# Kernel optimization log

Measured on AMD Instinct MI355X. Metric: run time of the kernel, lower is better.

## Reference

```python
import jax, jax.numpy as jnp
import numpy as np

B, S, D = 2, 2048, 1024
NH, HD = 16, 64
MLP = 4096
EPS = 1e-6  # flax nnx.RMSNorm default epsilon


def rms_norm(x, scale):
    var = jnp.mean(jnp.square(x.astype(jnp.float32)), axis=-1, keepdims=True)
    return (x * jax.lax.rsqrt(var + EPS)).astype(x.dtype) * scale


def setup_inputs() -> dict:
    key = jax.random.key(0)
    ks = jax.random.split(key, 16)
    lin = lambda k, fin, fout: jax.random.normal(k, (fin, fout), jnp.float32) / np.sqrt(fin)
    x = jax.random.normal(ks[0], (B, S, D), jnp.float32)
    # causal mask [b, s, s]
    mask = jnp.broadcast_to(jnp.tril(jnp.ones((S, S), jnp.bool_))[None], (B, S, S))
    return {
        "x": x,
        "mask": mask,
        "attn_norm_scale": jnp.ones((D,), jnp.float32),
        "q_w": lin(ks[1], D, D), "q_b": jnp.zeros((D,), jnp.float32),
        "k_w": lin(ks[2], D, D), "k_b": jnp.zeros((D,), jnp.float32),
        "v_w": lin(ks[3], D, D), "v_b": jnp.zeros((D,), jnp.float32),
        "o_w": lin(ks[4], D, D), "o_b": jnp.zeros((D,), jnp.float32),
        "ffn_norm_scale": jnp.ones((D,), jnp.float32),
        "gate_w": lin(ks[5], D, MLP), "gate_b": jnp.zeros((MLP,), jnp.float32),
        "up_w": lin(ks[6], D, MLP), "up_b": jnp.zeros((MLP,), jnp.float32),
        "down_w": lin(ks[7], MLP, D), "down_b": jnp.zeros((D,), jnp.float32),
    }


def reference(x, mask, attn_norm_scale, q_w, q_b, k_w, k_b, v_w, v_b, o_w, o_b,
              ffn_norm_scale, gate_w, gate_b, up_w, up_b, down_w, down_b):
    b, s, d = x.shape
    h = rms_norm(x, attn_norm_scale)
    q = (h @ q_w + q_b).reshape(b, s, NH, HD)
    k = (h @ k_w + k_b).reshape(b, s, NH, HD)
    v = (h @ v_w + v_b).reshape(b, s, NH, HD)
    scale = jnp.float32(HD) ** -0.5
    logits = jnp.einsum('bsnh,btnh->bnst', q, k) * scale  # [b, n, s, s]
    logits = jnp.where(mask[:, None, :, :], logits, jnp.finfo(logits.dtype).min)
    attn = jax.nn.softmax(logits.astype(jnp.float32), axis=-1).astype(x.dtype)
    attn_out = jnp.einsum('bnst,btnh->bsnh', attn, v).reshape(b, s, d)
    x = x + attn_out @ o_w + o_b
    h = rms_norm(x, ffn_norm_scale)
    ffn = (jax.nn.silu(h @ gate_w + gate_b) * (h @ up_w + up_b)) @ down_w + down_b
    return x + ffn
```

## Files before the change

kernel.cpp:

```cpp
#include <hip/hip_runtime.h>

#define S_LEN 2048
#define DMODEL 1024
#define NHEADS 16
#define MLPDIM 4096

typedef float f32x4 __attribute__((ext_vector_type(4)));
typedef __bf16 bf16x8 __attribute__((ext_vector_type(8)));
typedef __bf16 bf16x4 __attribute__((ext_vector_type(4)));

__device__ __forceinline__ void gload_lds16(const void* gsrc, void* ldst) {
  __builtin_amdgcn_global_load_lds(
      (const __attribute__((address_space(1))) void*)gsrc,
      (__attribute__((address_space(3))) void*)ldst, 16, 0, 0);
}

#define BARR() __builtin_amdgcn_s_barrier()
#define VMC(n) do { asm volatile("s_waitcnt vmcnt(" #n ")" ::: "memory"); __builtin_amdgcn_sched_barrier(0); } while (0)

__global__ __launch_bounds__(256) void transpose_cast64_k(
    const float* __restrict__ in, __bf16* __restrict__ out, int K, int N) {
  __shared__ __bf16 tile[64][66];
  int n0 = blockIdx.x * 64, k0 = blockIdx.y * 64;
  int t = threadIdx.x;
  int rr = (t & 63) >> 4, sl = t & 15, wv = t >> 6;
#pragma unroll
  for (int j = 0; j < 4; ++j) {
    int r = wv * 4 + rr + j * 16;
    f32x4 v = *(const f32x4*)(in + (size_t)(k0 + r) * N + n0 + sl * 4);
#pragma unroll
    for (int e = 0; e < 4; ++e) tile[r][sl * 4 + e] = (__bf16)v[e];
  }
  __syncthreads();
#pragma unroll
  for (int j = 0; j < 2; ++j) {
    int u = t + j * 256;
    int n = u >> 3, kc = u & 7;
    bf16x8 o;
#pragma unroll
    for (int e = 0; e < 8; ++e) o[e] = tile[kc * 8 + e][n];
    *(bf16x8*)(out + (size_t)(n0 + n) * K + k0 + kc * 8) = o;
  }
}

__global__ __launch_bounds__(256) void vtrans_k(
    const __bf16* __restrict__ qkv, __bf16* __restrict__ vt) {
  __shared__ __bf16 tile[32][33];
  int s0 = blockIdx.x * 32, c0 = blockIdx.y * 32, b = blockIdx.z;
  int tx = threadIdx.x & 31, ty = threadIdx.x >> 5;
#pragma unroll
  for (int r = 0; r < 32; r += 8)
    tile[r + ty][tx] = qkv[(size_t)(b * S_LEN + s0 + r + ty) * 3072 + 2048 + c0 + tx];
  __syncthreads();
#pragma unroll
  for (int r = 0; r < 32; r += 8)
    vt[(size_t)(b * 1024 + c0 + r + ty) * S_LEN + s0 + tx] = tile[tx][r + ty];
}

__global__ __launch_bounds__(256) void concat3_k(
    const float* __restrict__ a, const float* __restrict__ b,
    const float* __restrict__ c, float* __restrict__ dst) {
  int i = blockIdx.x * 256 + threadIdx.x;
  if (i < 1024) dst[i] = a[i];
  else if (i < 2048) dst[i] = b[i - 1024];
  else if (i < 3072) dst[i] = c[i - 2048];
}

__global__ __launch_bounds__(256) void rmsnorm_k(
    const float* __restrict__ x, const float* __restrict__ scale,
    __bf16* __restrict__ out) {
  int row = blockIdx.x, tid = threadIdx.x;
  f32x4 v = ((const f32x4*)(x + (size_t)row * DMODEL))[tid];
  float ss = v[0] * v[0] + v[1] * v[1] + v[2] * v[2] + v[3] * v[3];
#pragma unroll
  for (int off = 1; off < 64; off <<= 1) ss += __shfl_xor(ss, off, 64);
  __shared__ float part[4];
  if ((tid & 63) == 0) part[tid >> 6] = ss;
  __syncthreads();
  float tot = part[0] + part[1] + part[2] + part[3];
  float r = rsqrtf(tot * (1.0f / DMODEL) + 1e-6f);
  f32x4 s4 = ((const f32x4*)scale)[tid];
  bf16x4 o;
#pragma unroll
  for (int e = 0; e < 4; ++e) o[e] = (__bf16)(v[e] * r * s4[e]);
  ((bf16x4*)out)[(size_t)row * (DMODEL / 4) + tid] = o;
}

__global__ __launch_bounds__(256, 4) void gemm_gu(
    const __bf16* __restrict__ A, const __bf16* __restrict__ Gt,
    const __bf16* __restrict__ Ut, const float* __restrict__ gb,
    const float* __restrict__ ub, __bf16* __restrict__ Cout,
    int M, int N, int K) {
  __shared__ __attribute__((aligned(16))) __bf16 As[128 * 64];
  __shared__ __attribute__((aligned(16))) __bf16 Gs[64 * 64];
  __shared__ __attribute__((aligned(16))) __bf16 Us[64 * 64];
  int tid = threadIdx.x, lane = tid & 63, wave = tid >> 6;
  int l15 = lane & 15, g4 = lane >> 4;
  int lin = blockIdx.x;
  int xcd = lin & 7, idx = lin >> 3;
  int bxl = idx >> 4, byl = idx & 15;
  int bn = ((xcd & 3) * 16 + bxl) * 64;
  int bm = ((xcd >> 2) * 16 + byl) * 128;
  int wr = wave >> 1, wc = wave & 1;
  f32x4 ag[4][2] = {}, au[4][2] = {};
  const __bf16* Abase = A + (size_t)bm * K;
  const __bf16* Gbase = Gt + (size_t)bn * K;
  const __bf16* Ubase = Ut + (size_t)bn * K;

  for (int k0 = 0; k0 < K; k0 += 64) {
#pragma unroll
    for (int j = 0; j < 4; ++j) {
      int u = tid + j * 256;
      int r = u >> 3, c = (u & 7) ^ (r & 7);
      gload_lds16(Abase + (size_t)r * K + k0 + c * 8, As + u * 8);
    }
#pragma unroll
    for (int j = 0; j < 2; ++j) {
      int u = tid + j * 256;
      int r = u >> 3, c = (u & 7) ^ (r & 7);
      gload_lds16(Gbase + (size_t)r * K + k0 + c * 8, Gs + u * 8);
      gload_lds16(Ubase + (size_t)r * K + k0 + c * 8, Us + u * 8);
    }
    __syncthreads();
#pragma unroll
    for (int ks = 0; ks < 2; ++ks) {
      bf16x8 af[4], gf[2], uf[2];
#pragma unroll
      for (int m = 0; m < 4; ++m) {
        int r = wr * 64 + m * 16 + l15;
        af[m] = *(const bf16x8*)(As + r * 64 + (((4 * ks + g4) ^ (r & 7)) << 3));
      }
#pragma unroll
      for (int n = 0; n < 2; ++n) {
        int r = wc * 32 + n * 16 + l15;
        int off = r * 64 + (((4 * ks + g4) ^ (r & 7)) << 3);
        gf[n] = *(const bf16x8*)(Gs + off);
        uf[n] = *(const bf16x8*)(Us + off);
      }
      __builtin_amdgcn_s_setprio(1);
#pragma unroll
      for (int m = 0; m < 4; ++m)
#pragma unroll
        for (int n = 0; n < 2; ++n) {
          ag[m][n] = __builtin_amdgcn_mfma_f32_16x16x32_bf16(af[m], gf[n], ag[m][n], 0, 0, 0);
          au[m][n] = __builtin_amdgcn_mfma_f32_16x16x32_bf16(af[m], uf[n], au[m][n], 0, 0, 0);
        }
      __builtin_amdgcn_s_setprio(0);
    }
    __syncthreads();
  }
  int r0 = bm + wr * 64 + g4 * 4;
  int c0 = bn + wc * 32 + l15;
#pragma unroll
  for (int n = 0; n < 2; ++n) {
    int c = c0 + n * 16;
    float gbv = gb[c], ubv = ub[c];
#pragma unroll
    for (int m = 0; m < 4; ++m) {
      int rb = r0 + m * 16;
#pragma unroll
      for (int rg = 0; rg < 4; ++rg) {
        float g = ag[m][n][rg] + gbv;
        float u = au[m][n][rg] + ubv;
        float v = g / (1.0f + __expf(-g)) * u;
        Cout[(size_t)(rb + rg) * N + c] = (__bf16)v;
      }
    }
  }
}

template <int OUT_BF16, int RESID, int SILU>
__global__ __launch_bounds__(256, 3) void gemm_n64(
    const __bf16* __restrict__ A, const __bf16* __restrict__ Bt,
    const float* __restrict__ bias, const float* __restrict__ resid,
    const __bf16* __restrict__ aux, void* __restrict__ Cout,
    int M, int N, int K) {
  __shared__ __attribute__((aligned(16))) __bf16 As[2][128 * 64];
  __shared__ __attribute__((aligned(16))) __bf16 Bs[2][64 * 64];
  int tid = threadIdx.x, lane = tid & 63, wave = tid >> 6;
  int l15 = lane & 15, g4 = lane >> 4;
  int npx = M >> 10;
  int xcd = blockIdx.x & 7, j = blockIdx.x >> 3;
  int bm = (xcd * npx + (j % npx)) * 128;
  int bn = (j / npx) * 64;
  int wr = wave >> 1, wc = wave & 1;
  f32x4 acc[4][2] = {};
  const __bf16* Abase = A + (size_t)bm * K;
  const __bf16* Bbase = Bt + (size_t)bn * K;

  auto stage = [&](int k0, int sb) {
#pragma unroll
    for (int i = 0; i < 4; ++i) {
      int u = tid + i * 256;
      int r = u >> 3, c = (u & 7) ^ (r & 7);
      gload_lds16(Abase + (size_t)r * K + k0 + c * 8, As[sb] + u * 8);
    }
#pragma unroll
    for (int i = 0; i < 2; ++i) {
      int u = tid + i * 256;
      int r = u >> 3, c = (u & 7) ^ (r & 7);
      gload_lds16(Bbase + (size_t)r * K + k0 + c * 8, Bs[sb] + u * 8);
    }
  };

  int NT = K >> 6;
  stage(0, 0);
  for (int t = 0; t < NT; ++t) {
    int sb = t & 1;
    if (t + 1 < NT) { stage((t + 1) << 6, sb ^ 1); VMC(6); }
    else { VMC(0); }
    BARR();
#pragma unroll
    for (int ks = 0; ks < 2; ++ks) {
      bf16x8 af[4], bfr[2];
#pragma unroll
      for (int m = 0; m < 4; ++m) {
        int r = wr * 64 + m * 16 + l15;
        af[m] = *(const bf16x8*)(As[sb] + r * 64 + (((4 * ks + g4) ^ (r & 7)) << 3));
      }
#pragma unroll
      for (int n = 0; n < 2; ++n) {
        int r = wc * 32 + n * 16 + l15;
        bfr[n] = *(const bf16x8*)(Bs[sb] + r * 64 + (((4 * ks + g4) ^ (r & 7)) << 3));
      }
      __builtin_amdgcn_s_setprio(1);
#pragma unroll
      for (int m = 0; m < 4; ++m)
#pragma unroll
        for (int n = 0; n < 2; ++n)
          acc[m][n] = __builtin_amdgcn_mfma_f32_16x16x32_bf16(af[m], bfr[n], acc[m][n], 0, 0, 0);
      __builtin_amdgcn_s_setprio(0);
    }
    BARR();
  }
  int r0 = bm + wr * 64 + g4 * 4;
  int c0 = bn + wc * 32 + l15;
#pragma unroll
  for (int n = 0; n < 2; ++n) {
    int c = c0 + n * 16;
    float bv = bias[c];
#pragma unroll
    for (int m = 0; m < 4; ++m) {
      int rb = r0 + m * 16;
#pragma unroll
      for (int rg = 0; rg < 4; ++rg) {
        int r = rb + rg;
        size_t idx = (size_t)r * N + c;
        float v = acc[m][n][rg] + bv;
        if (SILU) {
          float gg = (float)aux[idx];
          v *= gg / (1.0f + __expf(-gg));
        }
        if (RESID) v += resid[idx];
        if (OUT_BF16) ((__bf16*)Cout)[idx] = (__bf16)v;
        else ((float*)Cout)[idx] = v;
      }
    }
  }
}

#define SCL2E 0.180336879f
__global__ __launch_bounds__(512, 4) void attn_k(
    const __bf16* __restrict__ qkv, const __bf16* __restrict__ vt,
    __bf16* __restrict__ ao) {
  __shared__ __attribute__((aligned(16))) __bf16 Ks[2][128 * 64];
  __shared__ __attribute__((aligned(16))) __bf16 Vs[2][64 * 128];
  int tid = threadIdx.x, lane = tid & 63, w = tid >> 6;
  int l15 = lane & 15, g4 = lane >> 4;
  int bh = blockIdx.x, b = bh >> 4, h = bh & 15;
  int qt = 15 - blockIdx.y;
  int qb = qt * 128;
  int qw = qb + w * 16;
  const __bf16* qkvb = qkv + (size_t)b * S_LEN * 3072 + h * 64;
  const __bf16* kgb = qkvb + 1024;
  const __bf16* vtb = vt + (size_t)b * 1024 * S_LEN + (size_t)(h * 64) * S_LEN;

  bf16x8 qf[2];
#pragma unroll
  for (int ks = 0; ks < 2; ++ks)
    qf[ks] = *(const bf16x8*)(qkvb + (size_t)(qw + l15) * 3072 + 32 * ks + 8 * g4);

  f32x4 oa[4] = {};
  float mrow = -1e30f, lrow = 0.f;
  int q = qw + l15;
  int nt = qt + 1;

  auto stage = [&](int kvb, int buf) {
#pragma unroll
    for (int i = 0; i < 2; ++i) {
      int u = tid + i * 512;
      int r = u >> 3, c = u & 7;
      gload_lds16(kgb + (size_t)(kvb + r) * 3072 + ((c ^ (r & 7)) << 3),
                  Ks[buf] + w * 512 + i * 4096);
    }
#pragma unroll
    for (int i = 0; i < 2; ++i) {
      int u = tid + i * 512;
      int r = u >> 4, cu = u & 15;
      gload_lds16(vtb + (size_t)r * S_LEN + kvb + ((cu ^ (r & 7)) << 3),
                  Vs[buf] + w * 512 + i * 4096);
    }
  };

  stage(0, 0);
  __syncthreads();
  int buf = 0;
  for (int t = 0; t < nt; ++t) {
    int kvb = t * 128;
    if (t + 1 < nt) stage(kvb + 128, buf ^ 1);

    f32x4 sa[8];
#pragma unroll
    for (int i = 0; i < 8; ++i) sa[i] = f32x4{0.f, 0.f, 0.f, 0.f};
#pragma unroll
    for (int st = 0; st < 2; ++st)
#pragma unroll
      for (int ks = 0; ks < 2; ++ks) {
        bf16x8 kf[4];
#pragma unroll
        for (int n = 0; n < 4; ++n) {
          int rr = st * 64 + n * 16 + l15;
          int bc = (64 * ks + 16 * g4) ^ ((rr & 7) << 4);
          kf[n] = *(const bf16x8*)((const char*)Ks[buf] + rr * 128 + bc);
        }
        __builtin_amdgcn_s_setprio(1);
#pragma unroll
        for (int n = 0; n < 4; ++n)
          sa[st * 4 + n] = __builtin_amdgcn_mfma_f32_16x16x32_bf16(kf[n], qf[ks], sa[st * 4 + n], 0, 0, 0);
        __builtin_amdgcn_s_setprio(0);
      }

    bool lastt = (t == nt - 1);
    float nmx = -1e30f;
#pragma unroll
    for (int i = 0; i < 8; ++i)
#pragma unroll
      for (int rg = 0; rg < 4; ++rg) {
        float s = sa[i][rg] * SCL2E;
        if (lastt) {
          int key = kvb + (i >> 2) * 64 + (i & 3) * 16 + 4 * g4 + rg;
          s = (key <= q) ? s : -1e30f;
        }
        sa[i][rg] = s;
        nmx = fmaxf(nmx, s);
      }
    nmx = fmaxf(nmx, __shfl_xor(nmx, 16));
    nmx = fmaxf(nmx, __shfl_xor(nmx, 32));
    float nm = fmaxf(mrow, nmx);
    float sc = exp2f(mrow - nm);
    mrow = nm;
    float rs = 0.f;
    bf16x8 pa[2][2];
#pragma unroll
    for (int st = 0; st < 2; ++st)
#pragma unroll
      for (int ks = 0; ks < 2; ++ks)
#pragma unroll
        for (int hf = 0; hf < 2; ++hf)
#pragma unroll
          for (int rg = 0; rg < 4; ++rg) {
            float p = exp2f(sa[st * 4 + 2 * ks + hf][rg] - nm);
            rs += p;
            pa[st][ks][hf * 4 + rg] = (__bf16)p;
          }
    rs += __shfl_xor(rs, 16);
    rs += __shfl_xor(rs, 32);
    lrow = lrow * sc + rs;
#pragma unroll
    for (int rg = 0; rg < 4; ++rg) {
      float scq = __shfl(sc, 4 * g4 + rg);
#pragma unroll
      for (int dn = 0; dn < 4; ++dn) oa[dn][rg] *= scq;
    }

#pragma unroll
    for (int st = 0; st < 2; ++st)
#pragma unroll
      for (int ks = 0; ks < 2; ++ks) {
        __builtin_amdgcn_s_setprio(1);
#pragma unroll
        for (int dn = 0; dn < 4; ++dn) {
          int rr = dn * 16 + l15;
          int swz = (rr & 7) << 4;
          int bb = st * 128 + 64 * ks + 8 * g4;
          const char* vrow = (const char*)Vs[buf] + rr * 256;
          bf16x4 v0 = *(const bf16x4*)(vrow + (bb ^ swz));
          bf16x4 v1 = *(const bf16x4*)(vrow + ((bb + 32) ^ swz));
          bf16x8 vf;
          vf[0] = v0[0]; vf[1] = v0[1]; vf[2] = v0[2]; vf[3] = v0[3];
          vf[4] = v1[0]; vf[5] = v1[1]; vf[6] = v1[2]; vf[7] = v1[3];
          oa[dn] = __builtin_amdgcn_mfma_f32_16x16x32_bf16(pa[st][ks], vf, oa[dn], 0, 0, 0);
        }
        __builtin_amdgcn_s_setprio(0);
      }
    __syncthreads();
    buf ^= 1;
  }

  __bf16* aobase = ao + (size_t)b * S_LEN * DMODEL + h * 64;
#pragma unroll
  for (int rg = 0; rg < 4; ++rg) {
    float rl = 1.0f / __shfl(lrow, 4 * g4 + rg);
    int qo = qw + 4 * g4 + rg;
#pragma unroll
    for (int dn = 0; dn < 4; ++dn)
      aobase[(size_t)qo * DMODEL + dn * 16 + l15] = (__bf16)(oa[dn][rg] * rl);
  }
}

#define OFF_WQKV 0
#define OFF_WO 6291456
#define OFF_WG 8388608
#define OFF_WU 16777216
#define OFF_WD 25165824
#define OFF_BQKV 33554432
#define OFF_H 33570816
#define OFF_QKV 41959424
#define OFF_AO 67125248
#define OFF_T 75513856
#define OFF_VT OFF_T
#define OFF_X2 109068288

extern "C" void kernel_launch(void* const* d_in, const int* in_sizes, int n_in,
                              void* d_out, int out_size, void* d_ws, size_t ws_size,
                              hipStream_t stream) {
  (void)in_sizes; (void)n_in; (void)out_size; (void)ws_size;
  const float* x = (const float*)d_in[0];
  const float* attn_scale = (const float*)d_in[2];
  const float* q_w = (const float*)d_in[3];
  const float* q_b = (const float*)d_in[4];
  const float* k_w = (const float*)d_in[5];
  const float* k_b = (const float*)d_in[6];
  const float* v_w = (const float*)d_in[7];
  const float* v_b = (const float*)d_in[8];
  const float* o_w = (const float*)d_in[9];
  const float* o_b = (const float*)d_in[10];
  const float* ffn_scale = (const float*)d_in[11];
  const float* gate_w = (const float*)d_in[12];
  const float* gate_b = (const float*)d_in[13];
  const float* up_w = (const float*)d_in[14];
  const float* up_b = (const float*)d_in[15];
  const float* down_w = (const float*)d_in[16];
  const float* down_b = (const float*)d_in[17];

  char* ws = (char*)d_ws;
  __bf16* wqkv = (__bf16*)(ws + OFF_WQKV);
  __bf16* wo = (__bf16*)(ws + OFF_WO);
  __bf16* wg = (__bf16*)(ws + OFF_WG);
  __bf16* wu = (__bf16*)(ws + OFF_WU);
  __bf16* wd = (__bf16*)(ws + OFF_WD);
  float* bqkv = (float*)(ws + OFF_BQKV);
  __bf16* hbuf = (__bf16*)(ws + OFF_H);
  __bf16* qkvbuf = (__bf16*)(ws + OFF_QKV);
  __bf16* aobuf = (__bf16*)(ws + OFF_AO);
  __bf16* tbuf = (__bf16*)(ws + OFF_T);
  __bf16* vtbuf = (__bf16*)(ws + OFF_VT);
  float* x2 = (float*)(ws + OFF_X2);

  dim3 blk(256);
  transpose_cast64_k<<<dim3(16, 16), blk, 0, stream>>>(q_w, wqkv, 1024, 1024);
  transpose_cast64_k<<<dim3(16, 16), blk, 0, stream>>>(k_w, wqkv + 1024 * 1024, 1024, 1024);
  transpose_cast64_k<<<dim3(16, 16), blk, 0, stream>>>(v_w, wqkv + 2 * 1024 * 1024, 1024, 1024);
  transpose_cast64_k<<<dim3(16, 16), blk, 0, stream>>>(o_w, wo, 1024, 1024);
  transpose_cast64_k<<<dim3(64, 16), blk, 0, stream>>>(gate_w, wg, 1024, 4096);
  transpose_cast64_k<<<dim3(64, 16), blk, 0, stream>>>(up_w, wu, 1024, 4096);
  transpose_cast64_k<<<dim3(16, 64), blk, 0, stream>>>(down_w, wd, 4096, 1024);
  concat3_k<<<12, blk, 0, stream>>>(q_b, k_b, v_b, bqkv);
  rmsnorm_k<<<4096, blk, 0, stream>>>(x, attn_scale, hbuf);
  gemm_n64<1, 0, 0><<<dim3(1536), blk, 0, stream>>>(hbuf, wqkv, bqkv, nullptr, nullptr, qkvbuf, 4096, 3072, 1024);
  vtrans_k<<<dim3(64, 32, 2), blk, 0, stream>>>(qkvbuf, vtbuf);
  attn_k<<<dim3(32, 16), dim3(512), 0, stream>>>(qkvbuf, vtbuf, aobuf);
  gemm_n64<0, 1, 0><<<dim3(512), blk, 0, stream>>>(aobuf, wo, o_b, x, nullptr, x2, 4096, 1024, 1024);
  rmsnorm_k<<<4096, blk, 0, stream>>>(x2, ffn_scale, hbuf);
  gemm_gu<<<dim3(2048), blk, 0, stream>>>(hbuf, wg, wu, gate_b, up_b, tbuf, 4096, 4096, 1024);
  gemm_n64<0, 1, 0><<<dim3(512), blk, 0, stream>>>(tbuf, wd, down_b, x2, nullptr, (float*)d_out, 4096, 1024, 4096);
}
```

Before: 271.4 us.

## Merge weight prep kernels, remap GEMM tile order, skip unneeded softmax rescale

Replaces eight separate weight transpose/cast and bias concat launches with one combined prep kernel, so fewer launches and the blocks of the small transposes can run concurrently. Changes the gemm_n64 block-to-tile mapping so that pairs of M-tiles share an N column within each XCD group, aiming at better L2 reuse. In attention, skips the exp2 rescale of the output accumulators and row sum when no row maximum increased anywhere in the wave. This adds a wave-wide vote and a branch per tile.

```diff
diff --git a/kernel.cpp b/kernel.cpp
--- a/kernel.cpp
+++ b/kernel.cpp
@@ -18,11 +18,44 @@
 #define BARR() __builtin_amdgcn_s_barrier()
 #define VMC(n) do { asm volatile("s_waitcnt vmcnt(" #n ")" ::: "memory"); __builtin_amdgcn_sched_barrier(0); } while (0)
 
-__global__ __launch_bounds__(256) void transpose_cast64_k(
-    const float* __restrict__ in, __bf16* __restrict__ out, int K, int N) {
+__global__ __launch_bounds__(256) void prep_k(
+    const float* __restrict__ qw, const float* __restrict__ kw,
+    const float* __restrict__ vw, const float* __restrict__ ow,
+    const float* __restrict__ gw, const float* __restrict__ uw,
+    const float* __restrict__ dw, __bf16* __restrict__ wqkv,
+    __bf16* __restrict__ wo, __bf16* __restrict__ wg, __bf16* __restrict__ wu,
+    __bf16* __restrict__ wd, const float* __restrict__ qb,
+    const float* __restrict__ kb, const float* __restrict__ vb,
+    float* __restrict__ bqkv) {
+  int bid = blockIdx.x, t = threadIdx.x;
+  if (bid >= 4096) {
+    int i = (bid - 4096) * 256 + t;
+    if (i < 1024) bqkv[i] = qb[i];
+    else if (i < 2048) bqkv[i] = kb[i - 1024];
+    else if (i < 3072) bqkv[i] = vb[i - 2048];
+    return;
+  }
+  const float* in;
+  __bf16* out;
+  int K, N, bx, by;
+  if (bid < 1024) {
+    int job = bid >> 8, tt = bid & 255;
+    K = 1024; N = 1024; bx = tt & 15; by = tt >> 4;
+    in = (job == 0) ? qw : (job == 1) ? kw : (job == 2) ? vw : ow;
+    out = (job == 0) ? wqkv : (job == 1) ? wqkv + 1024 * 1024
+        : (job == 2) ? wqkv + 2 * 1024 * 1024 : wo;
+  } else if (bid < 3072) {
+    int job = (bid - 1024) >> 10, tt = (bid - 1024) & 1023;
+    K = 1024; N = 4096; bx = tt & 63; by = tt >> 6;
+    in = job ? uw : gw;
+    out = job ? wu : wg;
+  } else {
+    int tt = bid - 3072;
+    K = 4096; N = 1024; bx = tt & 15; by = tt >> 4;
+    in = dw; out = wd;
+  }
   __shared__ __bf16 tile[64][66];
-  int n0 = blockIdx.x * 64, k0 = blockIdx.y * 64;
-  int t = threadIdx.x;
+  int n0 = bx * 64, k0 = by * 64;
   int rr = (t & 63) >> 4, sl = t & 15, wv = t >> 6;
 #pragma unroll
   for (int j = 0; j < 4; ++j) {
@@ -55,15 +88,6 @@
 #pragma unroll
   for (int r = 0; r < 32; r += 8)
     vt[(size_t)(b * 1024 + c0 + r + ty) * S_LEN + s0 + tx] = tile[tx][r + ty];
-}
-
-__global__ __launch_bounds__(256) void concat3_k(
-    const float* __restrict__ a, const float* __restrict__ b,
-    const float* __restrict__ c, float* __restrict__ dst) {
-  int i = blockIdx.x * 256 + threadIdx.x;
-  if (i < 1024) dst[i] = a[i];
-  else if (i < 2048) dst[i] = b[i - 1024];
-  else if (i < 3072) dst[i] = c[i - 2048];
 }
 
 __global__ __launch_bounds__(256) void rmsnorm_k(
@@ -179,10 +203,11 @@
   __shared__ __attribute__((aligned(16))) __bf16 Bs[2][64 * 64];
   int tid = threadIdx.x, lane = tid & 63, wave = tid >> 6;
   int l15 = lane & 15, g4 = lane >> 4;
-  int npx = M >> 10;
+  int NB = N >> 6;
   int xcd = blockIdx.x & 7, j = blockIdx.x >> 3;
-  int bm = (xcd * npx + (j % npx)) * 128;
-  int bn = (j / npx) * 64;
+  int grp = j / (2 * NB), jj = j - grp * 2 * NB;
+  int bm = (xcd * (M >> 10) + grp * 2 + (jj & 1)) * 128;
+  int bn = (jj >> 1) * 64;
   int wr = wave >> 1, wc = wave & 1;
   f32x4 acc[4][2] = {};
   const __bf16* Abase = A + (size_t)bm * K;
@@ -346,9 +371,21 @@
       }
     nmx = fmaxf(nmx, __shfl_xor(nmx, 16));
     nmx = fmaxf(nmx, __shfl_xor(nmx, 32));
-    float nm = fmaxf(mrow, nmx);
-    float sc = exp2f(mrow - nm);
-    mrow = nm;
+    float nm;
+    if (!__all(nmx <= mrow)) {
+      nm = fmaxf(mrow, nmx);
+      float sc = exp2f(mrow - nm);
+      mrow = nm;
+      lrow *= sc;
+#pragma unroll
+      for (int rg = 0; rg < 4; ++rg) {
+        float scq = __shfl(sc, 4 * g4 + rg);
+#pragma unroll
+        for (int dn = 0; dn < 4; ++dn) oa[dn][rg] *= scq;
+      }
+    } else {
+      nm = mrow;
+    }
     float rs = 0.f;
     bf16x8 pa[2][2];
 #pragma unroll
@@ -365,13 +402,7 @@
           }
     rs += __shfl_xor(rs, 16);
     rs += __shfl_xor(rs, 32);
-    lrow = lrow * sc + rs;
-#pragma unroll
-    for (int rg = 0; rg < 4; ++rg) {
-      float scq = __shfl(sc, 4 * g4 + rg);
-#pragma unroll
-      for (int dn = 0; dn < 4; ++dn) oa[dn][rg] *= scq;
-    }
+    lrow += rs;
 
 #pragma unroll
     for (int st = 0; st < 2; ++st)
@@ -458,14 +489,8 @@
   float* x2 = (float*)(ws + OFF_X2);
 
   dim3 blk(256);
-  transpose_cast64_k<<<dim3(16, 16), blk, 0, stream>>>(q_w, wqkv, 1024, 1024);
-  transpose_cast64_k<<<dim3(16, 16), blk, 0, stream>>>(k_w, wqkv + 1024 * 1024, 1024, 1024);
-  transpose_cast64_k<<<dim3(16, 16), blk, 0, stream>>>(v_w, wqkv + 2 * 1024 * 1024, 1024, 1024);
-  transpose_cast64_k<<<dim3(16, 16), blk, 0, stream>>>(o_w, wo, 1024, 1024);
-  transpose_cast64_k<<<dim3(64, 16), blk, 0, stream>>>(gate_w, wg, 1024, 4096);
-  transpose_cast64_k<<<dim3(64, 16), blk, 0, stream>>>(up_w, wu, 1024, 4096);
-  transpose_cast64_k<<<dim3(16, 64), blk, 0, stream>>>(down_w, wd, 4096, 1024);
-  concat3_k<<<12, blk, 0, stream>>>(q_b, k_b, v_b, bqkv);
+  prep_k<<<dim3(4108), blk, 0, stream>>>(q_w, k_w, v_w, o_w, gate_w, up_w, down_w,
+                                         wqkv, wo, wg, wu, wd, q_b, k_b, v_b, bqkv);
   rmsnorm_k<<<4096, blk, 0, stream>>>(x, attn_scale, hbuf);
   gemm_n64<1, 0, 0><<<dim3(1536), blk, 0, stream>>>(hbuf, wqkv, bqkv, nullptr, nullptr, qkvbuf, 4096, 3072, 1024);
   vtrans_k<<<dim3(64, 32, 2), blk, 0, stream>>>(qkvbuf, vtbuf);
```

Measured after the change: 257.0 us. 5.3% less time.
